# Kernel tuning notes

Hardware: AMD Instinct MI355X
Metric: run time of the kernel (lower is better)

Reference implementation:

```python
import jax, jax.numpy as jnp
import numpy as np

N = 50000        # nodes
E = 200000       # edges
D_IN = 128       # dim_input
D_E = 32         # dim_edge_features
D_H = 256        # dim_hidden
D_OUT = 256      # dim_output
N_LAYERS = 3
N_FRAG = 10000
N_GRAPH = 2000
BN_EPS = 1e-5
GINE_EPS = 0.0   # eps buffer, train_eps=False

_LAYER_DIMS = [(D_IN, D_H), (D_H, D_H), (D_H, D_OUT)]  # (node in, node out) per layer


def setup_inputs() -> dict:
    key = jax.random.key(0)
    ks = iter(jax.random.split(key, 64))
    inp = {}
    inp['x'] = jax.random.normal(next(ks), (N, D_IN), dtype=jnp.float32)
    inp['edge_attr'] = jax.random.normal(next(ks), (E, D_E), dtype=jnp.float32)
    inp['edge_index'] = jax.random.randint(next(ks), (2, E), 0, N, dtype=jnp.int64)
    inp['frag_batch'] = jnp.sort(jax.random.randint(next(ks), (N,), 0, N_FRAG, dtype=jnp.int64))
    inp['graph_batch'] = jnp.sort(jax.random.randint(next(ks), (N,), 0, N_GRAPH, dtype=jnp.int64))
    for i, (din, dout) in enumerate(_LAYER_DIMS):
        fin = din + D_E  # MLP input = node feat + edge feat (post-concat message)
        inp[f'w1_{i}'] = jax.random.normal(next(ks), (fin, D_H), dtype=jnp.float32) / np.sqrt(fin)
        inp[f'b1_{i}'] = jnp.zeros((D_H,), dtype=jnp.float32)
        inp[f'w2_{i}'] = jax.random.normal(next(ks), (D_H, dout), dtype=jnp.float32) / np.sqrt(D_H)
        inp[f'b2_{i}'] = jnp.zeros((dout,), dtype=jnp.float32)
        inp[f'g_{i}'] = jnp.ones((dout,), dtype=jnp.float32)     # BN weight
        inp[f'beta_{i}'] = jnp.zeros((dout,), dtype=jnp.float32)  # BN bias
    return inp


def _gine_layer(x, edge_attr, src, dst, w1, b1, w2, b2, g, beta):
    # message: relu(concat(x_j, e_ji)) gathered along edges  -> [E, din+De]
    m = jax.nn.relu(jnp.concatenate([x[src], edge_attr], axis=-1))
    # aggregate: scatter-add into target nodes -> [N, din+De]
    agg = jax.ops.segment_sum(m, dst, num_segments=N)
    # (1+eps)*x residual on the node-feature slice
    agg = agg.at[:, : x.shape[1]].add((1.0 + GINE_EPS) * x)
    # h_Theta MLP: Linear -> ReLU -> Linear
    h = jnp.dot(jax.nn.relu(jnp.dot(agg, w1) + b1), w2) + b2
    # ReLU then BatchNorm1d(track_running_stats=False): batch stats, biased var
    h = jax.nn.relu(h)
    mu = h.mean(axis=0)
    var = h.var(axis=0)
    return g * (h - mu) * jax.lax.rsqrt(var + BN_EPS) + beta


def _sqrt_pool(h, batch, num_segments):
    # nodes_per_graph, broadcast back per-node, sqrt-normalize, then add-pool
    cnt = jax.ops.segment_sum(jnp.ones((h.shape[0],), h.dtype), batch, num_segments=num_segments)
    inv_sqrt = jax.lax.rsqrt(jnp.maximum(cnt, 1.0))[batch]  # [N]
    return jax.ops.segment_sum(h * inv_sqrt[:, None], batch, num_segments=num_segments)


def reference(x, edge_attr, edge_index, frag_batch, graph_batch,
              w1_0, b1_0, w2_0, b2_0, g_0, beta_0,
              w1_1, b1_1, w2_1, b2_1, g_1, beta_1,
              w1_2, b1_2, w2_2, b2_2, g_2, beta_2):
    src, dst = edge_index[0], edge_index[1]
    params = [(w1_0, b1_0, w2_0, b2_0, g_0, beta_0),
              (w1_1, b1_1, w2_1, b2_1, g_1, beta_1),
              (w1_2, b1_2, w2_2, b2_2, g_2, beta_2)]
    h = x
    for p in params:
        h = _gine_layer(h, edge_attr, src, dst, *p)
    frag_out = _sqrt_pool(h, frag_batch, N_FRAG)    # [N_FRAG, D_OUT]
    graph_out = _sqrt_pool(h, graph_batch, N_GRAPH)  # [N_GRAPH, D_OUT]
    return (frag_out, graph_out)
```

## Files before the change

kernel.cpp:

```cpp
#include <hip/hip_runtime.h>

#define N_NODES 50000
#define N_EDGES 200000
#define DE 32
#define N_FRAG 10000
#define N_GRAPH 2000
#define BN_SLOTS 32
#define KSTR 296

typedef _Float16 f16x8 __attribute__((ext_vector_type(8)));
typedef _Float16 f16x4 __attribute__((ext_vector_type(4)));
typedef __attribute__((ext_vector_type(4))) float f32x4;

__device__ __forceinline__ float4 ld4(const float* p) { return *(const float4*)p; }
__device__ __forceinline__ float4 ld4(const _Float16* p) {
    f16x4 h = *(const f16x4*)p;
    float4 v; v.x = (float)h[0]; v.y = (float)h[1]; v.z = (float)h[2]; v.w = (float)h[3];
    return v;
}
__device__ __forceinline__ void st4h(_Float16* p, float4 v) {
    f16x4 h = {(_Float16)v.x, (_Float16)v.y, (_Float16)v.z, (_Float16)v.w};
    *(f16x4*)p = h;
}

__global__ __launch_bounds__(256)
void count_deg_kernel(const int* __restrict__ ei, int* __restrict__ deg) {
    int e = blockIdx.x * 256 + threadIdx.x;
    if (e < N_EDGES) atomicAdd(&deg[ei[N_EDGES + e]], 1);
}

__global__ __launch_bounds__(256)
void block_sum_kernel(const int* __restrict__ deg, int* __restrict__ bsum) {
    int i = blockIdx.x * 256 + threadIdx.x;
    int v = (i < N_NODES) ? deg[i] : 0;
#pragma unroll
    for (int o = 1; o < 64; o <<= 1) v += __shfl_xor(v, o);
    __shared__ int wsum[4];
    if ((threadIdx.x & 63) == 0) wsum[threadIdx.x >> 6] = v;
    __syncthreads();
    if (threadIdx.x == 0) bsum[blockIdx.x] = wsum[0] + wsum[1] + wsum[2] + wsum[3];
}

__global__ __launch_bounds__(256)
void top_scan_kernel(int* __restrict__ bsum, int nb) {
    __shared__ int s[256];
    int t = threadIdx.x;
    s[t] = (t < nb) ? bsum[t] : 0;
    __syncthreads();
    for (int o = 1; o < 256; o <<= 1) {
        int v = s[t];
        int a = (t >= o) ? s[t - o] : 0;
        __syncthreads();
        s[t] = v + a;
        __syncthreads();
    }
    if (t < nb) bsum[t] = (t > 0) ? s[t - 1] : 0;
}

__global__ __launch_bounds__(256)
void final_scan_kernel(const int* __restrict__ deg, const int* __restrict__ bsum,
                       int* __restrict__ ptr) {
    __shared__ int s[256];
    int i = blockIdx.x * 256 + threadIdx.x;
    int t = threadIdx.x;
    int v = (i < N_NODES) ? deg[i] : 0;
    s[t] = v;
    __syncthreads();
    for (int o = 1; o < 256; o <<= 1) {
        int x = s[t];
        int a = (t >= o) ? s[t - o] : 0;
        __syncthreads();
        s[t] = x + a;
        __syncthreads();
    }
    int incl = s[t];
    int base = bsum[blockIdx.x];
    if (i < N_NODES) ptr[i] = base + incl - v;
    if (i == N_NODES - 1) ptr[N_NODES] = base + incl;
}

__global__ __launch_bounds__(256)
void fill_csr_kernel(const int* __restrict__ ei, const int* __restrict__ row_ptr,
                     int* __restrict__ fill, int* __restrict__ csr_src,
                     int* __restrict__ csr_eid) {
    int e = blockIdx.x * 256 + threadIdx.x;
    if (e >= N_EDGES) return;
    int dst = ei[N_EDGES + e];
    int pos = row_ptr[dst] + atomicAdd(&fill[dst], 1);
    csr_src[pos] = ei[e];
    csr_eid[pos] = e;
}

__global__ __launch_bounds__(256)
void segptr2_kernel(const int* __restrict__ fb, const int* __restrict__ gb,
                    int* __restrict__ frag_ptr, int* __restrict__ graph_ptr) {
    int id = blockIdx.x * 256 + threadIdx.x;
    const int* batch;
    int* ptr;
    int s;
    if (id <= N_FRAG) { batch = fb; ptr = frag_ptr; s = id; }
    else if (id <= N_FRAG + 1 + N_GRAPH) { batch = gb; ptr = graph_ptr; s = id - (N_FRAG + 1); }
    else return;
    int lo = 0, hi = N_NODES;
    while (lo < hi) {
        int mid = (lo + hi) >> 1;
        if (batch[mid] < s) lo = mid + 1; else hi = mid;
    }
    ptr[s] = lo;
}

struct BsAll {
    const float* W[6];
    _Float16* BS[6];
    int base[7];
};

__global__ __launch_bounds__(256)
void bs16_all_kernel(BsAll a) {
    int id = blockIdx.x * 256 + threadIdx.x;
    if (id >= a.base[6]) return;
    int seg = 0;
#pragma unroll
    for (int i = 1; i < 6; ++i) seg += (id >= a.base[i]);
    int lid = id - a.base[seg];
    int j  = lid & 7;
    int l  = (lid >> 3) & 63;
    int cg = (lid >> 9) & 15;
    int kt = lid >> 13;
    int col = cg * 16 + (l & 15);
    int k   = kt * 32 + (l >> 4) * 8 + j;
    a.BS[seg][lid] = (_Float16)a.W[seg][(size_t)k * 256 + col];
}

__global__ __launch_bounds__(256)
void edge_gather_kernel(const float* __restrict__ ea, const int* __restrict__ row_ptr,
                        const int* __restrict__ csr_eid, float* __restrict__ agg_e) {
    int t = threadIdx.x;
    int g = t >> 3;
    int j = t & 7;
    int n = blockIdx.x * 32 + g;
    if (n >= N_NODES) return;
    int col = j << 2;
    float4 acc = {0.f, 0.f, 0.f, 0.f};
    int beg = row_ptr[n], end = row_ptr[n + 1];
    for (int e = beg; e < end; ++e) {
        int eid = csr_eid[e];
        float4 v = *(const float4*)(ea + (size_t)eid * DE + col);
        acc.x += fmaxf(v.x, 0.f);
        acc.y += fmaxf(v.y, 0.f);
        acc.z += fmaxf(v.z, 0.f);
        acc.w += fmaxf(v.w, 0.f);
    }
    *(float4*)(agg_e + (size_t)n * DE + col) = acc;
}

__global__ __launch_bounds__(256)
void relu16_f32_kernel(const float* __restrict__ x, _Float16* __restrict__ y) {
    size_t i = (size_t)(blockIdx.x * 256 + threadIdx.x) * 4;
    if (i >= (size_t)N_NODES * 128) return;
    float4 v = ld4(x + i);
    f16x4 o = {(_Float16)fmaxf(v.x, 0.f), (_Float16)fmaxf(v.y, 0.f),
               (_Float16)fmaxf(v.z, 0.f), (_Float16)fmaxf(v.w, 0.f)};
    *(f16x4*)(y + i) = o;
}

__global__ __launch_bounds__(256)
void bnrelu16_kernel(const _Float16* __restrict__ h, const float* __restrict__ sc,
                     const float* __restrict__ sh, _Float16* __restrict__ y) {
    size_t i = (size_t)(blockIdx.x * 256 + threadIdx.x) * 8;
    if (i >= (size_t)N_NODES * 256) return;
    int col = (int)(i & 255);
    f16x8 v = *(const f16x8*)(h + i);
    float4 s0 = ld4(sc + col), s1 = ld4(sc + col + 4);
    float4 t0 = ld4(sh + col), t1 = ld4(sh + col + 4);
    f16x8 o;
    o[0] = (_Float16)fmaxf(fmaf((float)v[0], s0.x, t0.x), 0.f);
    o[1] = (_Float16)fmaxf(fmaf((float)v[1], s0.y, t0.y), 0.f);
    o[2] = (_Float16)fmaxf(fmaf((float)v[2], s0.z, t0.z), 0.f);
    o[3] = (_Float16)fmaxf(fmaf((float)v[3], s0.w, t0.w), 0.f);
    o[4] = (_Float16)fmaxf(fmaf((float)v[4], s1.x, t1.x), 0.f);
    o[5] = (_Float16)fmaxf(fmaf((float)v[5], s1.y, t1.y), 0.f);
    o[6] = (_Float16)fmaxf(fmaf((float)v[6], s1.z, t1.z), 0.f);
    o[7] = (_Float16)fmaxf(fmaf((float)v[7], s1.w, t1.w), 0.f);
    *(f16x8*)(y + i) = o;
}

template <bool BNIN, typename T, int NC>
__global__ __launch_bounds__(512, 4)
void fused_mlp_kernel(const T* __restrict__ X, const _Float16* __restrict__ Yg,
                      const int* __restrict__ row_ptr, const int* __restrict__ csr_src,
                      const float* __restrict__ agg_e,
                      const float* __restrict__ bnsc, const float* __restrict__ bnsh,
                      const _Float16* __restrict__ B1, const float* __restrict__ bias1,
                      const _Float16* __restrict__ B2, const float* __restrict__ bias2,
                      _Float16* __restrict__ C, float* __restrict__ bnslot) {
    constexpr int DIN  = NC * 32;
    constexpr int K1   = DIN + 32;
    constexpr int NKT1 = K1 / 32;
    constexpr int CPT  = DIN / 8;
    constexpr int NV   = CPT / 8;
    __shared__ __align__(16) _Float16 sBuf[64 * KSTR];
    const int t = threadIdx.x;
    const int l = t & 63;
    const int w = t >> 6;
    const int lr = l & 15;
    const int lq = l >> 4;
    const int row0 = blockIdx.x << 6;
    const int cb = w << 5;

    {
        const int r = t >> 3, j = t & 7;
        const int jc = j << 3;
        const int gr = row0 + r;
        if (gr < N_NODES) {
            f16x8 acc16[NV];
#pragma unroll
            for (int c = 0; c < NV; ++c) acc16[c] = (f16x8){0, 0, 0, 0, 0, 0, 0, 0};
            const int beg = row_ptr[gr], end = row_ptr[gr + 1];
            for (int e = beg; e < end; ++e) {
                const _Float16* sp = Yg + (size_t)csr_src[e] * DIN + jc;
#pragma unroll
                for (int c = 0; c < NV; ++c) acc16[c] += *(const f16x8*)(sp + c * 64);
            }
            const T* xp = X + (size_t)gr * DIN + jc;
#pragma unroll
            for (int c = 0; c < NV; ++c) {
                float4 v0f = ld4(xp + c * 64);
                float4 v1f = ld4(xp + c * 64 + 4);
                if (BNIN) {
                    float4 sa = *(const float4*)(bnsc + c * 64 + jc);
                    float4 sb = *(const float4*)(bnsc + c * 64 + jc + 4);
                    float4 ta = *(const float4*)(bnsh + c * 64 + jc);
                    float4 tb = *(const float4*)(bnsh + c * 64 + jc + 4);
                    v0f.x = fmaf(v0f.x, sa.x, ta.x);
                    v0f.y = fmaf(v0f.y, sa.y, ta.y);
                    v0f.z = fmaf(v0f.z, sa.z, ta.z);
                    v0f.w = fmaf(v0f.w, sa.w, ta.w);
                    v1f.x = fmaf(v1f.x, sb.x, tb.x);
                    v1f.y = fmaf(v1f.y, sb.y, tb.y);
                    v1f.z = fmaf(v1f.z, sb.z, tb.z);
                    v1f.w = fmaf(v1f.w, sb.w, tb.w);
                }
                f16x8 o;
                o[0] = (_Float16)(v0f.x + (float)acc16[c][0]);
                o[1] = (_Float16)(v0f.y + (float)acc16[c][1]);
                o[2] = (_Float16)(v0f.z + (float)acc16[c][2]);
                o[3] = (_Float16)(v0f.w + (float)acc16[c][3]);
                o[4] = (_Float16)(v1f.x + (float)acc16[c][4]);
                o[5] = (_Float16)(v1f.y + (float)acc16[c][5]);
                o[6] = (_Float16)(v1f.z + (float)acc16[c][6]);
                o[7] = (_Float16)(v1f.w + (float)acc16[c][7]);
                *(f16x8*)&sBuf[r * KSTR + c * 64 + jc] = o;
            }
            float4 ev = *(const float4*)(agg_e + (size_t)gr * DE + (j << 2));
            st4h(&sBuf[r * KSTR + DIN + (j << 2)], ev);
        } else {
            f16x8 z8 = {0, 0, 0, 0, 0, 0, 0, 0};
#pragma unroll
            for (int c = 0; c < NV; ++c)
                *(f16x8*)&sBuf[r * KSTR + c * 64 + jc] = z8;
            f16x4 z4 = {0, 0, 0, 0};
            *(f16x4*)&sBuf[r * KSTR + DIN + (j << 2)] = z4;
        }
    }
    __syncthreads();

    f32x4 acc1[4][2];
#pragma unroll
    for (int mt = 0; mt < 4; ++mt)
#pragma unroll
        for (int nt = 0; nt < 2; ++nt) acc1[mt][nt] = (f32x4){0.f, 0.f, 0.f, 0.f};
#pragma unroll
    for (int kt = 0; kt < NKT1; ++kt) {
        f16x8 af[4], bf[2];
#pragma unroll
        for (int mt = 0; mt < 4; ++mt)
            af[mt] = *(const f16x8*)&sBuf[(mt * 16 + lr) * KSTR + (kt << 5) + (lq << 3)];
        const size_t bb = ((size_t)(kt * 16 + (w << 1))) * 512 + (l << 3);
#pragma unroll
        for (int nt = 0; nt < 2; ++nt)
            bf[nt] = *(const f16x8*)(B1 + bb + nt * 512);
#pragma unroll
        for (int mt = 0; mt < 4; ++mt)
#pragma unroll
            for (int nt = 0; nt < 2; ++nt)
                acc1[mt][nt] = __builtin_amdgcn_mfma_f32_16x16x32_f16(
                    af[mt], bf[nt], acc1[mt][nt], 0, 0, 0);
    }
    __syncthreads();

#pragma unroll
    for (int nt = 0; nt < 2; ++nt) {
        int col = cb + nt * 16 + lr;
        float bv = bias1[col];
#pragma unroll
        for (int mt = 0; mt < 4; ++mt)
#pragma unroll
            for (int i = 0; i < 4; ++i) {
                int rr = mt * 16 + lq * 4 + i;
                sBuf[rr * KSTR + col] = (_Float16)fmaxf(acc1[mt][nt][i] + bv, 0.f);
            }
    }
    __syncthreads();

    f32x4 acc2[4][2];
#pragma unroll
    for (int mt = 0; mt < 4; ++mt)
#pragma unroll
        for (int nt = 0; nt < 2; ++nt) acc2[mt][nt] = (f32x4){0.f, 0.f, 0.f, 0.f};
#pragma unroll
    for (int kt = 0; kt < 8; ++kt) {
        f16x8 af[4], bf[2];
#pragma unroll
        for (int mt = 0; mt < 4; ++mt)
            af[mt] = *(const f16x8*)&sBuf[(mt * 16 + lr) * KSTR + (kt << 5) + (lq << 3)];
        const size_t bb = ((size_t)(kt * 16 + (w << 1))) * 512 + (l << 3);
#pragma unroll
        for (int nt = 0; nt < 2; ++nt)
            bf[nt] = *(const f16x8*)(B2 + bb + nt * 512);
#pragma unroll
        for (int mt = 0; mt < 4; ++mt)
#pragma unroll
            for (int nt = 0; nt < 2; ++nt)
                acc2[mt][nt] = __builtin_amdgcn_mfma_f32_16x16x32_f16(
                    af[mt], bf[nt], acc2[mt][nt], 0, 0, 0);
    }
    __syncthreads();

    float* slot = bnslot + (size_t)(blockIdx.x & (BN_SLOTS - 1)) * 512;
#pragma unroll
    for (int nt = 0; nt < 2; ++nt) {
        int col = cb + nt * 16 + lr;
        float bv = bias2[col];
        float s = 0.f, qq = 0.f;
#pragma unroll
        for (int mt = 0; mt < 4; ++mt)
#pragma unroll
            for (int i = 0; i < 4; ++i) {
                int rr = mt * 16 + lq * 4 + i;
                float o = fmaxf(acc2[mt][nt][i] + bv, 0.f);
                sBuf[rr * KSTR + col] = (_Float16)o;
                if (row0 + rr < N_NODES) { s += o; qq += o * o; }
            }
        s += __shfl_xor(s, 16); s += __shfl_xor(s, 32);
        qq += __shfl_xor(qq, 16); qq += __shfl_xor(qq, 32);
        if (lq == 0) {
            atomicAdd(&slot[col], s);
            atomicAdd(&slot[256 + col], qq);
        }
    }
    __syncthreads();

#pragma unroll
    for (int k = 0; k < 4; ++k) {
        int rr  = (t >> 5) + k * 16;
        int col = (t & 31) * 8;
        int row = row0 + rr;
        if (row < N_NODES) {
            f16x8 v = *(const f16x8*)&sBuf[rr * KSTR + col];
            *(f16x8*)(C + (size_t)row * 256 + col) = v;
        }
    }
}

__global__ void bn_finalize_kernel(const float* __restrict__ slots,
                                   const float* __restrict__ g, const float* __restrict__ beta,
                                   float* __restrict__ scale, float* __restrict__ shift) {
    int c = threadIdx.x;
    float s = 0.f, q = 0.f;
    for (int k = 0; k < BN_SLOTS; ++k) {
        s += slots[(size_t)k * 512 + c];
        q += slots[(size_t)k * 512 + 256 + c];
    }
    float mu = s * (1.0f / N_NODES);
    float var = q * (1.0f / N_NODES) - mu * mu;
    float rstd = rsqrtf(var + 1e-5f);
    float sc = g[c] * rstd;
    scale[c] = sc;
    shift[c] = beta[c] - mu * sc;
}

__global__ __launch_bounds__(256)
void pool_seg_kernel(const _Float16* __restrict__ h, const int* __restrict__ ptr,
                     const float* __restrict__ bnsc, const float* __restrict__ bnsh,
                     float* __restrict__ out, int nseg) {
    int t = threadIdx.x;
    int g = t >> 6;
    int j = t & 63;
    int s = blockIdx.x * 4 + g;
    if (s >= nseg) return;
    int beg = ptr[s], end = ptr[s + 1];
    int col = j << 2;
    float4 sc = *(const float4*)(bnsc + col);
    float4 sh = *(const float4*)(bnsh + col);
    float4 acc = {0.f, 0.f, 0.f, 0.f};
    for (int i = beg; i < end; ++i) {
        float4 v = ld4(h + (size_t)i * 256 + col);
        acc.x += fmaf(v.x, sc.x, sh.x);
        acc.y += fmaf(v.y, sc.y, sh.y);
        acc.z += fmaf(v.z, sc.z, sh.z);
        acc.w += fmaf(v.w, sc.w, sh.w);
    }
    float w = rsqrtf(fmaxf((float)(end - beg), 1.0f));
    float4 o = {acc.x * w, acc.y * w, acc.z * w, acc.w * w};
    *(float4*)(out + (size_t)s * 256 + col) = o;
}

extern "C" void kernel_launch(void* const* d_in, const int* in_sizes, int n_in,
                              void* d_out, int out_size, void* d_ws, size_t ws_size,
                              hipStream_t stream) {
    const float* x  = (const float*)d_in[0];
    const float* ea = (const float*)d_in[1];
    const int*   ei = (const int*)d_in[2];
    const int*   fb = (const int*)d_in[3];
    const int*   gb = (const int*)d_in[4];
    const float* W1[3]   = {(const float*)d_in[5],  (const float*)d_in[11], (const float*)d_in[17]};
    const float* B1[3]   = {(const float*)d_in[6],  (const float*)d_in[12], (const float*)d_in[18]};
    const float* W2[3]   = {(const float*)d_in[7],  (const float*)d_in[13], (const float*)d_in[19]};
    const float* B2[3]   = {(const float*)d_in[8],  (const float*)d_in[14], (const float*)d_in[20]};
    const float* G[3]    = {(const float*)d_in[9],  (const float*)d_in[15], (const float*)d_in[21]};
    const float* BETA[3] = {(const float*)d_in[10], (const float*)d_in[16], (const float*)d_in[22]};

    const int FIN[3] = {160, 288, 288};
    const int NBLK = (N_NODES + 255) / 256;

    float* ws = (float*)d_ws;
    size_t off = 0;
    _Float16* bufA = (_Float16*)(ws + off); off += (size_t)N_NODES * 128;
    _Float16* bufB = (_Float16*)(ws + off); off += (size_t)N_NODES * 128;
    _Float16* ybuf = (_Float16*)(ws + off); off += (size_t)N_NODES * 128;
    float* agg_e = ws + off; off += (size_t)N_NODES * DE;
    float* bnss  = ws + off; off += 3 * 512;
    float* bnslots = ws + off; off += (size_t)3 * BN_SLOTS * 512;
    _Float16* w1f[3]; _Float16* w2f[3];
    {
        _Float16* sw = (_Float16*)(ws + off);
        _Float16* sw0 = sw;
        for (int l = 0; l < 3; ++l) { w1f[l] = sw; sw += 256 * FIN[l]; }
        for (int l = 0; l < 3; ++l) { w2f[l] = sw; sw += 256 * 256; }
        off += (size_t)(sw - sw0 + 1) / 2;
    }
    int* iw      = (int*)(ws + off);
    int* row_ptr = iw;                     iw += N_NODES + 1;
    int* deg     = iw;                     iw += N_NODES;
    int* fill    = iw;                     iw += N_NODES;
    int* csr_src = iw;                     iw += N_EDGES;
    int* csr_eid = iw;                     iw += N_EDGES;
    int* frag_ptr = iw;                    iw += N_FRAG + 1;
    int* graph_ptr = iw;                   iw += N_GRAPH + 1;
    int* bsum    = iw;                     iw += NBLK;

    hipMemsetAsync(deg, 0, 2 * N_NODES * sizeof(int), stream);
    hipMemsetAsync(bnslots, 0, (size_t)3 * BN_SLOTS * 512 * sizeof(float), stream);

    {
        BsAll a;
        a.W[0] = W1[0]; a.W[1] = W1[1]; a.W[2] = W1[2];
        a.W[3] = W2[0]; a.W[4] = W2[1]; a.W[5] = W2[2];
        a.BS[0] = w1f[0]; a.BS[1] = w1f[1]; a.BS[2] = w1f[2];
        a.BS[3] = w2f[0]; a.BS[4] = w2f[1]; a.BS[5] = w2f[2];
        int Ks[6] = {FIN[0], FIN[1], FIN[2], 256, 256, 256};
        int cum = 0;
        for (int i = 0; i < 6; ++i) { a.base[i] = cum; cum += Ks[i] * 256; }
        a.base[6] = cum;
        bs16_all_kernel<<<(cum + 255) / 256, 256, 0, stream>>>(a);
    }

    count_deg_kernel<<<(N_EDGES + 255) / 256, 256, 0, stream>>>(ei, deg);
    block_sum_kernel<<<NBLK, 256, 0, stream>>>(deg, bsum);
    top_scan_kernel<<<1, 256, 0, stream>>>(bsum, NBLK);
    final_scan_kernel<<<NBLK, 256, 0, stream>>>(deg, bsum, row_ptr);
    fill_csr_kernel<<<(N_EDGES + 255) / 256, 256, 0, stream>>>(ei, row_ptr, fill, csr_src, csr_eid);

    segptr2_kernel<<<(N_FRAG + N_GRAPH + 2 + 255) / 256, 256, 0, stream>>>(
        fb, gb, frag_ptr, graph_ptr);

    edge_gather_kernel<<<(N_NODES + 31) / 32, 256, 0, stream>>>(ea, row_ptr, csr_eid, agg_e);

    const int nblk_mlp = (N_NODES + 63) / 64;
    relu16_f32_kernel<<<(N_NODES * 128 / 4 + 255) / 256, 256, 0, stream>>>(x, ybuf);
    {
        float* slotsL = bnslots;
        fused_mlp_kernel<false, float, 4><<<nblk_mlp, 512, 0, stream>>>(
            x, ybuf, row_ptr, csr_src, agg_e, nullptr, nullptr,
            w1f[0], B1[0], w2f[0], B2[0], bufA, slotsL);
        bn_finalize_kernel<<<1, 256, 0, stream>>>(slotsL, G[0], BETA[0], bnss, bnss + 256);
    }
    {
        float* slotsL = bnslots + (size_t)1 * BN_SLOTS * 512;
        const float* psc = bnss, * psh = bnss + 256;
        bnrelu16_kernel<<<(N_NODES * 256 / 8 + 255) / 256, 256, 0, stream>>>(bufA, psc, psh, ybuf);
        fused_mlp_kernel<true, _Float16, 8><<<nblk_mlp, 512, 0, stream>>>(
            bufA, ybuf, row_ptr, csr_src, agg_e, psc, psh,
            w1f[1], B1[1], w2f[1], B2[1], bufB, slotsL);
        bn_finalize_kernel<<<1, 256, 0, stream>>>(slotsL, G[1], BETA[1], bnss + 512, bnss + 768);
    }
    {
        float* slotsL = bnslots + (size_t)2 * BN_SLOTS * 512;
        const float* psc = bnss + 512, * psh = bnss + 768;
        bnrelu16_kernel<<<(N_NODES * 256 / 8 + 255) / 256, 256, 0, stream>>>(bufB, psc, psh, ybuf);
        fused_mlp_kernel<true, _Float16, 8><<<nblk_mlp, 512, 0, stream>>>(
            bufB, ybuf, row_ptr, csr_src, agg_e, psc, psh,
            w1f[2], B1[2], w2f[2], B2[2], bufA, slotsL);
        bn_finalize_kernel<<<1, 256, 0, stream>>>(slotsL, G[2], BETA[2], bnss + 1024, bnss + 1280);
    }

    const float* fsc = bnss + 2 * 512;
    const float* fsh = fsc + 256;
    pool_seg_kernel<<<(N_FRAG + 3) / 4, 256, 0, stream>>>(bufA, frag_ptr, fsc, fsh,
                                                          (float*)d_out, N_FRAG);
    pool_seg_kernel<<<(N_GRAPH + 3) / 4, 256, 0, stream>>>(bufA, graph_ptr, fsc, fsh,
                                                           (float*)d_out + (size_t)N_FRAG * 256, N_GRAPH);
}
```

Baseline: 355.0 us.

## Fuse BN finalize into bnrelu, merge pooling launches, prefetch neighbor gathers

Result: no change. 349.1 us (-1.7%).

```diff
diff --git a/kernel.cpp b/kernel.cpp
--- a/kernel.cpp
+++ b/kernel.cpp
@@ -143,13 +143,21 @@
     int col = j << 2;
     float4 acc = {0.f, 0.f, 0.f, 0.f};
     int beg = row_ptr[n], end = row_ptr[n + 1];
-    for (int e = beg; e < end; ++e) {
-        int eid = csr_eid[e];
-        float4 v = *(const float4*)(ea + (size_t)eid * DE + col);
-        acc.x += fmaxf(v.x, 0.f);
-        acc.y += fmaxf(v.y, 0.f);
-        acc.z += fmaxf(v.z, 0.f);
-        acc.w += fmaxf(v.w, 0.f);
+    int e = beg;
+    float4 va, vb;
+    if (e < end) va = *(const float4*)(ea + (size_t)csr_eid[e] * DE + col);
+    while (e + 2 <= end) {
+        vb = *(const float4*)(ea + (size_t)csr_eid[e + 1] * DE + col);
+        acc.x += fmaxf(va.x, 0.f); acc.y += fmaxf(va.y, 0.f);
+        acc.z += fmaxf(va.z, 0.f); acc.w += fmaxf(va.w, 0.f);
+        if (e + 2 < end) va = *(const float4*)(ea + (size_t)csr_eid[e + 2] * DE + col);
+        acc.x += fmaxf(vb.x, 0.f); acc.y += fmaxf(vb.y, 0.f);
+        acc.z += fmaxf(vb.z, 0.f); acc.w += fmaxf(vb.w, 0.f);
+        e += 2;
+    }
+    if (e < end) {
+        acc.x += fmaxf(va.x, 0.f); acc.y += fmaxf(va.y, 0.f);
+        acc.z += fmaxf(va.z, 0.f); acc.w += fmaxf(va.w, 0.f);
     }
     *(float4*)(agg_e + (size_t)n * DE + col) = acc;
 }
@@ -165,24 +173,39 @@
 }
 
 __global__ __launch_bounds__(256)
-void bnrelu16_kernel(const _Float16* __restrict__ h, const float* __restrict__ sc,
-                     const float* __restrict__ sh, _Float16* __restrict__ y) {
-    size_t i = (size_t)(blockIdx.x * 256 + threadIdx.x) * 8;
-    if (i >= (size_t)N_NODES * 256) return;
-    int col = (int)(i & 255);
-    f16x8 v = *(const f16x8*)(h + i);
-    float4 s0 = ld4(sc + col), s1 = ld4(sc + col + 4);
-    float4 t0 = ld4(sh + col), t1 = ld4(sh + col + 4);
-    f16x8 o;
-    o[0] = (_Float16)fmaxf(fmaf((float)v[0], s0.x, t0.x), 0.f);
-    o[1] = (_Float16)fmaxf(fmaf((float)v[1], s0.y, t0.y), 0.f);
-    o[2] = (_Float16)fmaxf(fmaf((float)v[2], s0.z, t0.z), 0.f);
-    o[3] = (_Float16)fmaxf(fmaf((float)v[3], s0.w, t0.w), 0.f);
-    o[4] = (_Float16)fmaxf(fmaf((float)v[4], s1.x, t1.x), 0.f);
-    o[5] = (_Float16)fmaxf(fmaf((float)v[5], s1.y, t1.y), 0.f);
-    o[6] = (_Float16)fmaxf(fmaf((float)v[6], s1.z, t1.z), 0.f);
-    o[7] = (_Float16)fmaxf(fmaf((float)v[7], s1.w, t1.w), 0.f);
-    *(f16x8*)(y + i) = o;
+void bnfin_relu16_kernel(const float* __restrict__ slots,
+                         const float* __restrict__ g, const float* __restrict__ beta,
+                         const _Float16* __restrict__ h, _Float16* __restrict__ y,
+                         float* __restrict__ scale_out, float* __restrict__ shift_out) {
+    __shared__ float ssc[256], ssh[256];
+    const int t = threadIdx.x;
+    {
+        float s = 0.f, q = 0.f;
+        for (int k = 0; k < BN_SLOTS; ++k) {
+            s += slots[(size_t)k * 512 + t];
+            q += slots[(size_t)k * 512 + 256 + t];
+        }
+        float mu = s * (1.0f / N_NODES);
+        float var = q * (1.0f / N_NODES) - mu * mu;
+        float rstd = rsqrtf(var + 1e-5f);
+        float sc = g[t] * rstd;
+        float sh = beta[t] - mu * sc;
+        ssc[t] = sc; ssh[t] = sh;
+        if (blockIdx.x == 0) { scale_out[t] = sc; shift_out[t] = sh; }
+    }
+    __syncthreads();
+    const size_t total = (size_t)N_NODES * 256 / 8;
+    for (size_t idx = (size_t)blockIdx.x * 256 + t; idx < total;
+         idx += (size_t)gridDim.x * 256) {
+        size_t i = idx * 8;
+        int col = (int)(i & 255);
+        f16x8 v = *(const f16x8*)(h + i);
+        f16x8 o;
+#pragma unroll
+        for (int k2 = 0; k2 < 8; ++k2)
+            o[k2] = (_Float16)fmaxf(fmaf((float)v[k2], ssc[col + k2], ssh[col + k2]), 0.f);
+        *(f16x8*)(y + i) = o;
+    }
 }
 
 template <bool BNIN, typename T, int NC>
@@ -217,10 +240,33 @@
 #pragma unroll
             for (int c = 0; c < NV; ++c) acc16[c] = (f16x8){0, 0, 0, 0, 0, 0, 0, 0};
             const int beg = row_ptr[gr], end = row_ptr[gr + 1];
-            for (int e = beg; e < end; ++e) {
+            int e = beg;
+            f16x8 va[NV], vb[NV];
+            if (e < end) {
                 const _Float16* sp = Yg + (size_t)csr_src[e] * DIN + jc;
 #pragma unroll
-                for (int c = 0; c < NV; ++c) acc16[c] += *(const f16x8*)(sp + c * 64);
+                for (int c = 0; c < NV; ++c) va[c] = *(const f16x8*)(sp + c * 64);
+            }
+            while (e + 2 <= end) {
+                {
+                    const _Float16* sp = Yg + (size_t)csr_src[e + 1] * DIN + jc;
+#pragma unroll
+                    for (int c = 0; c < NV; ++c) vb[c] = *(const f16x8*)(sp + c * 64);
+                }
+#pragma unroll
+                for (int c = 0; c < NV; ++c) acc16[c] += va[c];
+                if (e + 2 < end) {
+                    const _Float16* sp = Yg + (size_t)csr_src[e + 2] * DIN + jc;
+#pragma unroll
+                    for (int c = 0; c < NV; ++c) va[c] = *(const f16x8*)(sp + c * 64);
+                }
+#pragma unroll
+                for (int c = 0; c < NV; ++c) acc16[c] += vb[c];
+                e += 2;
+            }
+            if (e < end) {
+#pragma unroll
+                for (int c = 0; c < NV; ++c) acc16[c] += va[c];
             }
             const T* xp = X + (size_t)gr * DIN + jc;
 #pragma unroll
@@ -381,13 +427,19 @@
 }
 
 __global__ __launch_bounds__(256)
-void pool_seg_kernel(const _Float16* __restrict__ h, const int* __restrict__ ptr,
-                     const float* __restrict__ bnsc, const float* __restrict__ bnsh,
-                     float* __restrict__ out, int nseg) {
+void pool_both_kernel(const _Float16* __restrict__ h,
+                      const int* __restrict__ frag_ptr, const int* __restrict__ graph_ptr,
+                      const float* __restrict__ bnsc, const float* __restrict__ bnsh,
+                      float* __restrict__ out) {
+    const int NFB = (N_FRAG + 3) / 4;
+    int b = blockIdx.x;
+    const int* ptr; float* o; int nseg; int sb;
+    if (b < NFB) { ptr = frag_ptr; o = out; nseg = N_FRAG; sb = b * 4; }
+    else { ptr = graph_ptr; o = out + (size_t)N_FRAG * 256; nseg = N_GRAPH; sb = (b - NFB) * 4; }
     int t = threadIdx.x;
     int g = t >> 6;
     int j = t & 63;
-    int s = blockIdx.x * 4 + g;
+    int s = sb + g;
     if (s >= nseg) return;
     int beg = ptr[s], end = ptr[s + 1];
     int col = j << 2;
@@ -402,8 +454,8 @@
         acc.w += fmaf(v.w, sc.w, sh.w);
     }
     float w = rsqrtf(fmaxf((float)(end - beg), 1.0f));
-    float4 o = {acc.x * w, acc.y * w, acc.z * w, acc.w * w};
-    *(float4*)(out + (size_t)s * 256 + col) = o;
+    float4 ov = {acc.x * w, acc.y * w, acc.z * w, acc.w * w};
+    *(float4*)(o + (size_t)s * 256 + col) = ov;
 }
 
 extern "C" void kernel_launch(void* const* d_in, const int* in_sizes, int n_in,
@@ -479,36 +531,26 @@
 
     const int nblk_mlp = (N_NODES + 63) / 64;
     relu16_f32_kernel<<<(N_NODES * 128 / 4 + 255) / 256, 256, 0, stream>>>(x, ybuf);
-    {
-        float* slotsL = bnslots;
-        fused_mlp_kernel<false, float, 4><<<nblk_mlp, 512, 0, stream>>>(
-            x, ybuf, row_ptr, csr_src, agg_e, nullptr, nullptr,
-            w1f[0], B1[0], w2f[0], B2[0], bufA, slotsL);
-        bn_finalize_kernel<<<1, 256, 0, stream>>>(slotsL, G[0], BETA[0], bnss, bnss + 256);
-    }
-    {
-        float* slotsL = bnslots + (size_t)1 * BN_SLOTS * 512;
-        const float* psc = bnss, * psh = bnss + 256;
-        bnrelu16_kernel<<<(N_NODES * 256 / 8 + 255) / 256, 256, 0, stream>>>(bufA, psc, psh, ybuf);
-        fused_mlp_kernel<true, _Float16, 8><<<nblk_mlp, 512, 0, stream>>>(
-            bufA, ybuf, row_ptr, csr_src, agg_e, psc, psh,
-            w1f[1], B1[1], w2f[1], B2[1], bufB, slotsL);
-        bn_finalize_kernel<<<1, 256, 0, stream>>>(slotsL, G[1], BETA[1], bnss + 512, bnss + 768);
-    }
-    {
-        float* slotsL = bnslots + (size_t)2 * BN_SLOTS * 512;
-        const float* psc = bnss + 512, * psh = bnss + 768;
-        bnrelu16_kernel<<<(N_NODES * 256 / 8 + 255) / 256, 256, 0, stream>>>(bufB, psc, psh, ybuf);
-        fused_mlp_kernel<true, _Float16, 8><<<nblk_mlp, 512, 0, stream>>>(
-            bufB, ybuf, row_ptr, csr_src, agg_e, psc, psh,
-            w1f[2], B1[2], w2f[2], B2[2], bufA, slotsL);
-        bn_finalize_kernel<<<1, 256, 0, stream>>>(slotsL, G[2], BETA[2], bnss + 1024, bnss + 1280);
-    }
-
-    const float* fsc = bnss + 2 * 512;
-    const float* fsh = fsc + 256;
-    pool_seg_kernel<<<(N_FRAG + 3) / 4, 256, 0, stream>>>(bufA, frag_ptr, fsc, fsh,
-                                                          (float*)d_out, N_FRAG);
-    pool_seg_kernel<<<(N_GRAPH + 3) / 4, 256, 0, stream>>>(bufA, graph_ptr, fsc, fsh,
-                                                           (float*)d_out + (size_t)N_FRAG * 256, N_GRAPH);
-}
+    fused_mlp_kernel<false, float, 4><<<nblk_mlp, 512, 0, stream>>>(
+        x, ybuf, row_ptr, csr_src, agg_e, nullptr, nullptr,
+        w1f[0], B1[0], w2f[0], B2[0], bufA, bnslots);
+
+    bnfin_relu16_kernel<<<1024, 256, 0, stream>>>(
+        bnslots, G[0], BETA[0], bufA, ybuf, bnss, bnss + 256);
+    fused_mlp_kernel<true, _Float16, 8><<<nblk_mlp, 512, 0, stream>>>(
+        bufA, ybuf, row_ptr, csr_src, agg_e, bnss, bnss + 256,
+        w1f[1], B1[1], w2f[1], B2[1], bufB, bnslots + (size_t)1 * BN_SLOTS * 512);
+
+    bnfin_relu16_kernel<<<1024, 256, 0, stream>>>(
+        bnslots + (size_t)1 * BN_SLOTS * 512, G[1], BETA[1], bufB, ybuf,
+        bnss + 512, bnss + 768);
+    fused_mlp_kernel<true, _Float16, 8><<<nblk_mlp, 512, 0, stream>>>(
+        bufB, ybuf, row_ptr, csr_src, agg_e, bnss + 512, bnss + 768,
+        w1f[2], B1[2], w2f[2], B2[2], bufA, bnslots + (size_t)2 * BN_SLOTS * 512);
+
+    bn_finalize_kernel<<<1, 256, 0, stream>>>(
+        bnslots + (size_t)2 * BN_SLOTS * 512, G[2], BETA[2], bnss + 1024, bnss + 1280);
+    const int NFB = (N_FRAG + 3) / 4, NGB = (N_GRAPH + 3) / 4;
+    pool_both_kernel<<<NFB + NGB, 256, 0, stream>>>(
+        bufA, frag_ptr, graph_ptr, bnss + 1024, bnss + 1280, (float*)d_out);
+}
```
